# Optimization experiments

Hardware: AMD Instinct MI355X
Metric: run time of the kernel (lower is better)

The kernel has to match this reference:

```python
import jax, jax.numpy as jnp
import numpy as np

B, N, E, H = 2, 50000, 400000, 128


def _lin_init(k, fan_in, fan_out):
    s = 1.0 / np.sqrt(fan_in)
    kw, kb = jax.random.split(k)
    W = jax.random.uniform(kw, (fan_in, fan_out), jnp.float32, -s, s)
    b = jax.random.uniform(kb, (fan_out,), jnp.float32, -s, s)
    return W, b


def setup_inputs() -> dict:
    key = jax.random.key(0)
    ks = jax.random.split(key, 7)
    x = jax.random.normal(ks[0], (B, N, H), jnp.float32)
    edge_index = jax.random.randint(ks[1], (2, E), 0, N, jnp.int64)
    edge_attr = jax.random.normal(ks[2], (B, E, H), jnp.float32)
    We1, be1 = _lin_init(ks[3], 3 * H, H)
    We2, be2 = _lin_init(ks[4], H, H)
    Wn1, bn1 = _lin_init(ks[5], 2 * H, H)
    Wn2, bn2 = _lin_init(ks[6], H, H)
    return dict(x=x, edge_index=edge_index, edge_attr=edge_attr,
                We1=We1, be1=be1, We2=We2, be2=be2,
                Wn1=Wn1, bn1=bn1, Wn2=Wn2, bn2=bn2)


def reference(x, edge_index, edge_attr, We1, be1, We2, be2, Wn1, bn1, Wn2, bn2):
    src = edge_index[0]
    dest = edge_index[1]
    # edge model: MLP(concat(src_feat, dest_feat, edge_attr))  [B,E,3H] -> [B,E,H]
    m = jnp.concatenate([x[:, src], x[:, dest], edge_attr], axis=-1)
    e = jax.nn.relu(m @ We1 + be1) @ We2 + be2
    # node model: scatter-sum messages to dest nodes, then MLP(concat(x, agg))
    agg = jax.vmap(lambda eb: jax.ops.segment_sum(eb, dest, num_segments=x.shape[1]))(e)
    h = jnp.concatenate([x, agg], axis=-1)  # [B,N,2H]
    x_out = jax.nn.relu(h @ Wn1 + bn1) @ Wn2 + bn2
    return x_out, e
```

## Files before the change

### kernel.cpp

```cpp
#include <hip/hip_runtime.h>
#include <hip/hip_bf16.h>

#define Hd 128
#define Nn 50000
#define Ee 400000
#define Bb 2
#define NROWS 100000
#define TPB2 3125
#define NT2 6250

typedef __attribute__((ext_vector_type(8))) short bf16x8;
typedef __attribute__((ext_vector_type(4))) short bf16x4;
typedef __attribute__((ext_vector_type(4))) float f32x4;

static __device__ __forceinline__ short f2bf(float f) {
    __hip_bfloat16 h = __float2bfloat16(f);
    return *reinterpret_cast<short*>(&h);
}
static __device__ __forceinline__ float bf2f(short s) {
    union { unsigned u; float f; } v; v.u = ((unsigned)(unsigned short)s) << 16;
    return v.f;
}
static __device__ __forceinline__ bf16x8 cvt8(float4 a, float4 b) {
    bf16x8 r;
    r[0] = f2bf(a.x); r[1] = f2bf(a.y); r[2] = f2bf(a.z); r[3] = f2bf(a.w);
    r[4] = f2bf(b.x); r[5] = f2bf(b.y); r[6] = f2bf(b.z); r[7] = f2bf(b.w);
    return r;
}
static __device__ __forceinline__ unsigned pk2(float a, float b) {
    return (unsigned)(unsigned short)f2bf(a) | ((unsigned)(unsigned short)f2bf(b) << 16);
}
static __device__ __forceinline__ void lds_barrier() {
    asm volatile("s_waitcnt lgkmcnt(0)" ::: "memory");
    __builtin_amdgcn_s_barrier();
}

__global__ void prep_weights(const float* __restrict__ We1, const float* __restrict__ We2,
                             const float* __restrict__ Wn1, const float* __restrict__ Wn2,
                             short* __restrict__ wbuf) {
    int gid = blockIdx.x * 256 + threadIdx.x;
    if (gid < 32768) {
        int c = gid >> 7, k = gid & 127;
        float v = (c < 128) ? We1[k * 128 + c] : We1[(k + 128) * 128 + (c - 128)];
        wbuf[gid] = f2bf(v); return;
    }
    int g = gid - 32768;
    if (g < 16384) { int c = g >> 7, k = g & 127; wbuf[gid] = f2bf(We1[(k + 256) * 128 + c]); return; }
    g -= 16384;
    if (g < 16384) { int c = g >> 7, k = g & 127; wbuf[gid] = f2bf(We2[k * 128 + c]); return; }
    g -= 16384;
    if (g < 32768) { int c = g >> 8, k = g & 255; wbuf[gid] = f2bf(Wn1[k * 128 + c]); return; }
    g -= 32768;
    if (g < 16384) { int c = g >> 7, k = g & 127; wbuf[gid] = f2bf(Wn2[k * 128 + c]); }
}

__global__ void hist_kernel(const int* __restrict__ ei, int* __restrict__ cnt) {
    int t = blockIdx.x * 256 + threadIdx.x;
    if (t < Ee) atomicAdd(&cnt[ei[Ee + t]], 1);
}
__global__ void scan1(const int* __restrict__ cnt, int* __restrict__ cur, int* __restrict__ part) {
    __shared__ int s[256];
    int i = blockIdx.x * 256 + threadIdx.x;
    int v = (i < Nn) ? cnt[i] : 0;
    s[threadIdx.x] = v; __syncthreads();
    #pragma unroll
    for (int off = 1; off < 256; off <<= 1) {
        int u = (threadIdx.x >= off) ? s[threadIdx.x - off] : 0;
        __syncthreads(); s[threadIdx.x] += u; __syncthreads();
    }
    if (i < Nn) cur[i] = s[threadIdx.x] - v;
    if (threadIdx.x == 255) part[blockIdx.x] = s[255];
}
__global__ void scan2(int* __restrict__ part) {
    if (threadIdx.x == 0 && blockIdx.x == 0) {
        int run = 0;
        for (int i = 0; i < 196; i++) { int t = part[i]; part[i] = run; run += t; }
    }
}
__global__ void scan3(int* __restrict__ cur, const int* __restrict__ part) {
    int i = blockIdx.x * 256 + threadIdx.x;
    if (i < Nn) cur[i] += part[blockIdx.x];
}
__global__ void scatter_k(const int* __restrict__ ei, int* __restrict__ cur, int* __restrict__ elist) {
    int t = blockIdx.x * 256 + threadIdx.x;
    if (t < Ee) { int d = ei[Ee + t]; int pos = atomicAdd(&cur[d], 1); elist[pos] = t; }
}

__global__ __launch_bounds__(256) void node_pre(
    const float* __restrict__ x, const short* __restrict__ WabT,
    short* __restrict__ xa, short* __restrict__ xb)
{
    __shared__ __align__(16) short X[32 * 128];

    const int nbase = blockIdx.x * 32;
    const int t = threadIdx.x;
    const int wv = t >> 6, lane = t & 63;
    const int row16 = lane & 15, kg = lane >> 4;

    {
        int g = t >> 3, q = t & 7;
        const float* src = x + ((size_t)(nbase + g)) * Hd + q * 16;
        float4 a0 = ((const float4*)src)[0], a1 = ((const float4*)src)[1];
        float4 a2 = ((const float4*)src)[2], a3 = ((const float4*)src)[3];
        ((bf16x8*)X)[g * 16 + ((q * 2) ^ (g & 7))]     = cvt8(a0, a1);
        ((bf16x8*)X)[g * 16 + ((q * 2 + 1) ^ (g & 7))] = cvt8(a2, a3);
    }

    bf16x8 wf[4][4];
    #pragma unroll
    for (int nt = 0; nt < 4; nt++) {
        int n = wv * 64 + nt * 16 + row16;
        #pragma unroll
        for (int kt = 0; kt < 4; kt++)
            wf[kt][nt] = *(const bf16x8*)(WabT + n * 128 + kt * 32 + kg * 8);
    }
    __syncthreads();

    f32x4 acc[2][4];
    #pragma unroll
    for (int mt = 0; mt < 2; mt++)
        #pragma unroll
        for (int nt = 0; nt < 4; nt++) acc[mt][nt] = (f32x4){0.f,0.f,0.f,0.f};

    #pragma unroll
    for (int mt = 0; mt < 2; mt++) {
        int row = mt * 16 + row16;
        #pragma unroll
        for (int kt = 0; kt < 4; kt++) {
            bf16x8 xf = ((const bf16x8*)X)[row * 16 + ((kt * 4 + kg) ^ (row & 7))];
            #pragma unroll
            for (int nt = 0; nt < 4; nt++)
                acc[mt][nt] = __builtin_amdgcn_mfma_f32_16x16x32_bf16(wf[kt][nt], xf, acc[mt][nt], 0, 0, 0);
        }
    }

    #pragma unroll
    for (int mt = 0; mt < 2; mt++) {
        size_t node = nbase + mt * 16 + row16;
        #pragma unroll
        for (int nt = 0; nt < 4; nt++) {
            int ch = wv * 64 + nt * 16 + kg * 4;
            uint2 pk = { pk2(acc[mt][nt][0], acc[mt][nt][1]), pk2(acc[mt][nt][2], acc[mt][nt][3]) };
            short* dst = (ch < 128) ? (xa + node * Hd + ch) : (xb + node * Hd + (ch - 128));
            *(uint2*)dst = pk;
        }
    }
}

__global__ __launch_bounds__(512) void edge_mlp(
    const float* __restrict__ ea, const int* __restrict__ ei,
    const int* __restrict__ elist,
    const short* __restrict__ xa, const short* __restrict__ xb,
    const short* __restrict__ W1cT, const float* __restrict__ be1,
    const short* __restrict__ W2T, const float* __restrict__ be2,
    float* __restrict__ e_out, float* __restrict__ agg)
{
    __shared__ __align__(16) char smem[65536 + 1536];
    short* Aea = (short*)smem;
    short* A2  = (short*)(smem + 32768);
    int* ol = (int*)(smem + 65536);
    int* sl = ol + 128;
    int* dl = sl + 128;

    const int orig = blockIdx.x;
    const int q = NT2 / 8, rr = NT2 % 8;
    const int xcd = orig & 7, idx = orig >> 3;
    const int tile = (xcd < rr ? xcd * (q + 1) : rr * (q + 1) + (xcd - rr) * q) + idx;

    const int b = tile / TPB2;
    const int w0 = (tile % TPB2) * 128;
    const int t = threadIdx.x;
    const int wv = t >> 6, lane = t & 63;
    const int row16 = lane & 15, kg = lane >> 4;
    const int n0 = wv * 16 + kg * 4;
    const int sr = t >> 3, sq = t & 7;

    if (t < 128) {
        int o = elist[w0 + t];
        ol[t] = o; sl[t] = ei[o]; dl[t] = ei[Ee + o];
    }
    __syncthreads();

    int on[8], sn[8], dn[8];
    #pragma unroll
    for (int mt = 0; mt < 8; mt++) {
        int r = mt * 16 + row16;
        on[mt] = ol[r]; sn[mt] = sl[r]; dn[mt] = dl[r];
    }

    #pragma unroll
    for (int h = 0; h < 2; h++) {
        int row = sr + h * 64;
        const float* src = ea + ((size_t)b * Ee + ol[row]) * Hd + sq * 16;
        float4 a0 = ((const float4*)src)[0], a1 = ((const float4*)src)[1];
        float4 a2 = ((const float4*)src)[2], a3 = ((const float4*)src)[3];
        ((bf16x8*)Aea)[row * 16 + ((sq * 2) ^ (row & 7))]     = cvt8(a0, a1);
        ((bf16x8*)Aea)[row * 16 + ((sq * 2 + 1) ^ (row & 7))] = cvt8(a2, a3);
    }

    bf16x8 w1[4], w2[4];
    {
        const short* wp1 = W1cT + (wv * 16 + row16) * 128 + kg * 8;
        const short* wp2 = W2T  + (wv * 16 + row16) * 128 + kg * 8;
        #pragma unroll
        for (int kt = 0; kt < 4; kt++) {
            w1[kt] = *(const bf16x8*)(wp1 + kt * 32);
            w2[kt] = *(const bf16x8*)(wp2 + kt * 32);
        }
    }
    bf16x4 av[8], bv[8];
    #pragma unroll
    for (int mt = 0; mt < 8; mt++) {
        av[mt] = *(const bf16x4*)(xa + ((size_t)b * Nn + sn[mt]) * Hd + n0);
        bv[mt] = *(const bf16x4*)(xb + ((size_t)b * Nn + dn[mt]) * Hd + n0);
    }
    const float4 b1v = *(const float4*)(be1 + n0);
    const float4 b2v = *(const float4*)(be2 + n0);
    lds_barrier();

    f32x4 acc[8];
    #pragma unroll
    for (int mt = 0; mt < 8; mt++) acc[mt] = (f32x4){0.f,0.f,0.f,0.f};
    #pragma unroll
    for (int kt = 0; kt < 4; kt++) {
        #pragma unroll
        for (int mt = 0; mt < 8; mt++) {
            int row = mt * 16 + row16;
            bf16x8 af = ((const bf16x8*)Aea)[row * 16 + ((kt * 4 + kg) ^ (row & 7))];
            acc[mt] = __builtin_amdgcn_mfma_f32_16x16x32_bf16(w1[kt], af, acc[mt], 0, 0, 0);
        }
    }

    #pragma unroll
    for (int mt = 0; mt < 8; mt++) {
        int row = mt * 16 + row16;
        float vv[4];
        #pragma unroll
        for (int r = 0; r < 4; r++) {
            float u = acc[mt][r] + b1v[r] + bf2f(av[mt][r]) + bf2f(bv[mt][r]);
            vv[r] = u > 0.f ? u : 0.f;
        }
        int G = (n0 >> 3) ^ (row & 7);
        *(uint2*)((char*)A2 + row * 256 + G * 16 + (n0 & 7) * 2) =
            (uint2){ pk2(vv[0], vv[1]), pk2(vv[2], vv[3]) };
    }
    lds_barrier();

    #pragma unroll
    for (int mt = 0; mt < 8; mt++) acc[mt] = (f32x4){0.f,0.f,0.f,0.f};
    #pragma unroll
    for (int kt = 0; kt < 4; kt++) {
        #pragma unroll
        for (int mt = 0; mt < 8; mt++) {
            int row = mt * 16 + row16;
            bf16x8 hf = *(const bf16x8*)((const char*)A2 + row * 256 + (((kt * 4 + kg) ^ (row & 7)) * 16));
            acc[mt] = __builtin_amdgcn_mfma_f32_16x16x32_bf16(w2[kt], hf, acc[mt], 0, 0, 0);
        }
    }

    #pragma unroll
    for (int mt = 0; mt < 8; mt++) {
        acc[mt][0] += b2v.x; acc[mt][1] += b2v.y;
        acc[mt][2] += b2v.z; acc[mt][3] += b2v.w;
        float4 ov = { acc[mt][0], acc[mt][1], acc[mt][2], acc[mt][3] };
        *(float4*)(e_out + ((size_t)b * Ee + on[mt]) * Hd + n0) = ov;
    }
    lds_barrier();

    #pragma unroll
    for (int mt = 0; mt < 8; mt++) {
        int row = mt * 16 + row16;
        float4 ov = { acc[mt][0], acc[mt][1], acc[mt][2], acc[mt][3] };
        *(float4*)(smem + row * 512 + (((n0 >> 2) ^ (row & 7)) << 4)) = ov;
    }
    lds_barrier();

    {
        int c = t & 127, rg2 = t >> 7;
        int g_c = c >> 2, sub = (c & 3) << 2;
        int base = rg2 * 32;
        float s = 0.f;
        int pd = dl[base];
        #pragma unroll
        for (int i = 0; i < 32; i++) {
            int row = base + i;
            float v = *(const float*)(smem + row * 512 + ((g_c ^ (row & 7)) << 4) + sub);
            int d = dl[row];
            if (d != pd) {
                unsafeAtomicAdd(agg + ((size_t)b * Nn + pd) * Hd + c, s);
                s = 0.f; pd = d;
            }
            s += v;
        }
        unsafeAtomicAdd(agg + ((size_t)b * Nn + pd) * Hd + c, s);
    }
}

__global__ __launch_bounds__(512, 4) void node_mlp(
    const float* __restrict__ x, const float* __restrict__ agg,
    const short* __restrict__ Wn1T, const float* __restrict__ bn1,
    const short* __restrict__ Wn2T, const float* __restrict__ bn2,
    float* __restrict__ xout)
{
    __shared__ __align__(16) short A[32 * 256];
    __shared__ __align__(16) short A2[32 * 128];

    const int tilesPerB = (Nn + 31) / 32;
    const int bid = blockIdx.x;
    const int b = bid / tilesPerB;
    const int nbase = (bid % tilesPerB) * 32;
    const int t = threadIdx.x;
    const int wv = t >> 6, lane = t & 63;
    const int row16 = lane & 15, kg = lane >> 4;
    const int n0 = wv * 16 + kg * 4;

    {
        int g = t >> 4, q2 = t & 15;
        int n = nbase + g;
        float4 xv0 = {0,0,0,0}, xv1 = xv0;
        float4 s0 = {0,0,0,0}, s1 = s0;
        if (n < Nn) {
            const float* xr = x + ((size_t)b * Nn + n) * Hd + q2 * 8;
            xv0 = ((const float4*)xr)[0]; xv1 = ((const float4*)xr)[1];
            const float* ar = agg + ((size_t)b * Nn + n) * Hd + q2 * 8;
            s0 = ((const float4*)ar)[0]; s1 = ((const float4*)ar)[1];
        }
        ((bf16x8*)A)[g * 32 + (q2 ^ (g & 7))]        = cvt8(xv0, xv1);
        ((bf16x8*)A)[g * 32 + ((16 + q2) ^ (g & 7))] = cvt8(s0, s1);
    }

    bf16x8 w1[8];
    {
        const short* wp = Wn1T + (wv * 16 + row16) * 256 + kg * 8;
        #pragma unroll
        for (int kt = 0; kt < 8; kt++) w1[kt] = *(const bf16x8*)(wp + kt * 32);
    }
    __syncthreads();

    f32x4 acc[2];
    acc[0] = (f32x4){0.f,0.f,0.f,0.f}; acc[1] = (f32x4){0.f,0.f,0.f,0.f};
    #pragma unroll
    for (int kt = 0; kt < 8; kt++) {
        #pragma unroll
        for (int mt = 0; mt < 2; mt++) {
            int row = mt * 16 + row16;
            bf16x8 af = ((const bf16x8*)A)[row * 32 + ((kt * 4 + kg) ^ (row & 7))];
            acc[mt] = __builtin_amdgcn_mfma_f32_16x16x32_bf16(w1[kt], af, acc[mt], 0, 0, 0);
        }
    }

    float4 b1v = *(const float4*)(bn1 + n0);
    bf16x8 w2[4];
    {
        const short* wp = Wn2T + (wv * 16 + row16) * 128 + kg * 8;
        #pragma unroll
        for (int kt = 0; kt < 4; kt++) w2[kt] = *(const bf16x8*)(wp + kt * 32);
    }

    #pragma unroll
    for (int mt = 0; mt < 2; mt++) {
        int row = mt * 16 + row16;
        float v[4];
        #pragma unroll
        for (int r = 0; r < 4; r++) {
            float u = acc[mt][r] + b1v[r];
            v[r] = u > 0.f ? u : 0.f;
        }
        int G = (n0 >> 3) ^ (row & 7);
        *(uint2*)((char*)A2 + row * 256 + G * 16 + (n0 & 7) * 2) = (uint2){ pk2(v[0], v[1]), pk2(v[2], v[3]) };
    }
    __syncthreads();

    f32x4 acc2[2];
    acc2[0] = (f32x4){0.f,0.f,0.f,0.f}; acc2[1] = (f32x4){0.f,0.f,0.f,0.f};
    #pragma unroll
    for (int kt = 0; kt < 4; kt++) {
        #pragma unroll
        for (int mt = 0; mt < 2; mt++) {
            int row = mt * 16 + row16;
            bf16x8 hf = *(const bf16x8*)((const char*)A2 + row * 256 + (((kt * 4 + kg) ^ (row & 7)) * 16));
            acc2[mt] = __builtin_amdgcn_mfma_f32_16x16x32_bf16(w2[kt], hf, acc2[mt], 0, 0, 0);
        }
    }
    float4 b2v = *(const float4*)(bn2 + n0);
    #pragma unroll
    for (int mt = 0; mt < 2; mt++) {
        int node = nbase + mt * 16 + row16;
        if (node < Nn) {
            float4 ov;
            ov.x = acc2[mt][0] + b2v.x;
            ov.y = acc2[mt][1] + b2v.y;
            ov.z = acc2[mt][2] + b2v.z;
            ov.w = acc2[mt][3] + b2v.w;
            *(float4*)(xout + ((size_t)b * Nn + node) * Hd + n0) = ov;
        }
    }
}

extern "C" void kernel_launch(void* const* d_in, const int* in_sizes, int n_in,
                              void* d_out, int out_size, void* d_ws, size_t ws_size,
                              hipStream_t stream) {
    const float* x   = (const float*)d_in[0];
    const int*   ei  = (const int*)d_in[1];
    const float* ea  = (const float*)d_in[2];
    const float* We1 = (const float*)d_in[3];
    const float* be1 = (const float*)d_in[4];
    const float* We2 = (const float*)d_in[5];
    const float* be2 = (const float*)d_in[6];
    const float* Wn1 = (const float*)d_in[7];
    const float* bn1 = (const float*)d_in[8];
    const float* Wn2 = (const float*)d_in[9];
    const float* bn2 = (const float*)d_in[10];

    float* xout  = (float*)d_out;
    float* e_out = xout + (size_t)Bb * Nn * Hd;

    char* w = (char*)d_ws;
    short* wbuf  = (short*)w;
    short* xa    = (short*)(w + 229376);
    short* xb    = xa + (size_t)NROWS * Hd;
    float* agg   = (float*)(xb + (size_t)NROWS * Hd);
    int*   cnt   = (int*)(agg + (size_t)Bb * Nn * Hd);
    int*   cur   = cnt + Nn;
    int*   part  = cur + Nn;
    int*   elist = part + 256;

    hipMemsetAsync(cnt, 0, Nn * sizeof(int), stream);
    hipMemsetAsync(agg, 0, (size_t)Bb * Nn * Hd * sizeof(float), stream);

    prep_weights<<<448, 256, 0, stream>>>(We1, We2, Wn1, Wn2, wbuf);
    hist_kernel<<<(Ee + 255) / 256, 256, 0, stream>>>(ei, cnt);
    scan1<<<196, 256, 0, stream>>>(cnt, cur, part);
    scan2<<<1, 64, 0, stream>>>(part);
    scan3<<<196, 256, 0, stream>>>(cur, part);
    scatter_k<<<(Ee + 255) / 256, 256, 0, stream>>>(ei, cur, elist);

    node_pre<<<NROWS / 32, 256, 0, stream>>>(x, wbuf, xa, xb);

    edge_mlp<<<NT2, 512, 0, stream>>>(
        ea, ei, elist, xa, xb, wbuf + 32768, be1, wbuf + 49152, be2, e_out, agg);

    node_mlp<<<Bb * ((Nn + 31) / 32), 512, 0, stream>>>(
        x, agg, wbuf + 65536, bn1, wbuf + 98304, bn2, xout);
}
```

Before: 453.8 us.

## Fuse scan stages into scatter and enlarge node MLP tile to 64 rows

Replaces the serial single-thread partial-sum scan with a parallel block scan and folds the block-offset add into the scatter kernel, removing one launch and a pass over the counts. The node MLP now processes 64 nodes per block instead of 32, so each wave's register-held weight fragments are reused across twice as many MFMA tiles and fewer blocks are launched. The larger tile doubles shared memory per block and accumulator registers, and the occupancy hint on launch_bounds is dropped. Out-of-range node loads are clamped rather than zero-filled.

```diff
diff --git a/kernel.cpp b/kernel.cpp
--- a/kernel.cpp
+++ b/kernel.cpp
@@ -72,18 +72,25 @@
     if (threadIdx.x == 255) part[blockIdx.x] = s[255];
 }
 __global__ void scan2(int* __restrict__ part) {
-    if (threadIdx.x == 0 && blockIdx.x == 0) {
-        int run = 0;
-        for (int i = 0; i < 196; i++) { int t = part[i]; part[i] = run; run += t; }
-    }
-}
-__global__ void scan3(int* __restrict__ cur, const int* __restrict__ part) {
-    int i = blockIdx.x * 256 + threadIdx.x;
-    if (i < Nn) cur[i] += part[blockIdx.x];
-}
-__global__ void scatter_k(const int* __restrict__ ei, int* __restrict__ cur, int* __restrict__ elist) {
+    __shared__ int s[256];
+    int i = threadIdx.x;
+    int v = (i < 196) ? part[i] : 0;
+    s[i] = v; __syncthreads();
+    #pragma unroll
+    for (int off = 1; off < 256; off <<= 1) {
+        int u = (i >= off) ? s[i - off] : 0;
+        __syncthreads(); s[i] += u; __syncthreads();
+    }
+    if (i < 196) part[i] = s[i] - v;
+}
+__global__ void scatter_k(const int* __restrict__ ei, int* __restrict__ cur,
+                          const int* __restrict__ part, int* __restrict__ elist) {
     int t = blockIdx.x * 256 + threadIdx.x;
-    if (t < Ee) { int d = ei[Ee + t]; int pos = atomicAdd(&cur[d], 1); elist[pos] = t; }
+    if (t < Ee) {
+        int d = ei[Ee + t];
+        int pos = part[d >> 8] + atomicAdd(&cur[d], 1);
+        elist[pos] = t;
+    }
 }
 
 __global__ __launch_bounds__(256) void node_pre(
@@ -296,37 +303,38 @@
     }
 }
 
-__global__ __launch_bounds__(512, 4) void node_mlp(
+__global__ __launch_bounds__(512) void node_mlp(
     const float* __restrict__ x, const float* __restrict__ agg,
     const short* __restrict__ Wn1T, const float* __restrict__ bn1,
     const short* __restrict__ Wn2T, const float* __restrict__ bn2,
     float* __restrict__ xout)
 {
-    __shared__ __align__(16) short A[32 * 256];
-    __shared__ __align__(16) short A2[32 * 128];
-
-    const int tilesPerB = (Nn + 31) / 32;
+    __shared__ __align__(16) short A[64 * 256];
+    __shared__ __align__(16) short A2[64 * 128];
+
+    const int tilesPerB = (Nn + 63) / 64;
     const int bid = blockIdx.x;
     const int b = bid / tilesPerB;
-    const int nbase = (bid % tilesPerB) * 32;
+    const int nbase = (bid % tilesPerB) * 64;
     const int t = threadIdx.x;
     const int wv = t >> 6, lane = t & 63;
     const int row16 = lane & 15, kg = lane >> 4;
     const int n0 = wv * 16 + kg * 4;
 
     {
-        int g = t >> 4, q2 = t & 15;
+        int g = t >> 3, q = t & 7;
         int n = nbase + g;
-        float4 xv0 = {0,0,0,0}, xv1 = xv0;
-        float4 s0 = {0,0,0,0}, s1 = s0;
-        if (n < Nn) {
-            const float* xr = x + ((size_t)b * Nn + n) * Hd + q2 * 8;
-            xv0 = ((const float4*)xr)[0]; xv1 = ((const float4*)xr)[1];
-            const float* ar = agg + ((size_t)b * Nn + n) * Hd + q2 * 8;
-            s0 = ((const float4*)ar)[0]; s1 = ((const float4*)ar)[1];
-        }
-        ((bf16x8*)A)[g * 32 + (q2 ^ (g & 7))]        = cvt8(xv0, xv1);
-        ((bf16x8*)A)[g * 32 + ((16 + q2) ^ (g & 7))] = cvt8(s0, s1);
+        int nc_ = n < Nn ? n : Nn - 1;
+        const float* xr = x + ((size_t)b * Nn + nc_) * Hd + q * 16;
+        float4 x0 = ((const float4*)xr)[0], x1 = ((const float4*)xr)[1];
+        float4 x2 = ((const float4*)xr)[2], x3 = ((const float4*)xr)[3];
+        const float* ar = agg + ((size_t)b * Nn + nc_) * Hd + q * 16;
+        float4 s0 = ((const float4*)ar)[0], s1 = ((const float4*)ar)[1];
+        float4 s2 = ((const float4*)ar)[2], s3 = ((const float4*)ar)[3];
+        ((bf16x8*)A)[g * 32 + ((q * 2) ^ (g & 7))]          = cvt8(x0, x1);
+        ((bf16x8*)A)[g * 32 + ((q * 2 + 1) ^ (g & 7))]      = cvt8(x2, x3);
+        ((bf16x8*)A)[g * 32 + ((16 + q * 2) ^ (g & 7))]     = cvt8(s0, s1);
+        ((bf16x8*)A)[g * 32 + ((16 + q * 2 + 1) ^ (g & 7))] = cvt8(s2, s3);
     }
 
     bf16x8 w1[8];
@@ -335,21 +343,22 @@
         #pragma unroll
         for (int kt = 0; kt < 8; kt++) w1[kt] = *(const bf16x8*)(wp + kt * 32);
     }
-    __syncthreads();
-
-    f32x4 acc[2];
-    acc[0] = (f32x4){0.f,0.f,0.f,0.f}; acc[1] = (f32x4){0.f,0.f,0.f,0.f};
+    const float4 b1v = *(const float4*)(bn1 + n0);
+    lds_barrier();
+
+    f32x4 acc[4];
+    #pragma unroll
+    for (int mt = 0; mt < 4; mt++) acc[mt] = (f32x4){0.f,0.f,0.f,0.f};
     #pragma unroll
     for (int kt = 0; kt < 8; kt++) {
         #pragma unroll
-        for (int mt = 0; mt < 2; mt++) {
+        for (int mt = 0; mt < 4; mt++) {
             int row = mt * 16 + row16;
             bf16x8 af = ((const bf16x8*)A)[row * 32 + ((kt * 4 + kg) ^ (row & 7))];
             acc[mt] = __builtin_amdgcn_mfma_f32_16x16x32_bf16(w1[kt], af, acc[mt], 0, 0, 0);
         }
     }
 
-    float4 b1v = *(const float4*)(bn1 + n0);
     bf16x8 w2[4];
     {
         const short* wp = Wn2T + (wv * 16 + row16) * 128 + kg * 8;
@@ -358,7 +367,7 @@
     }
 
     #pragma unroll
-    for (int mt = 0; mt < 2; mt++) {
+    for (int mt = 0; mt < 4; mt++) {
         int row = mt * 16 + row16;
         float v[4];
         #pragma unroll
@@ -369,29 +378,29 @@
         int G = (n0 >> 3) ^ (row & 7);
         *(uint2*)((char*)A2 + row * 256 + G * 16 + (n0 & 7) * 2) = (uint2){ pk2(v[0], v[1]), pk2(v[2], v[3]) };
     }
-    __syncthreads();
-
-    f32x4 acc2[2];
-    acc2[0] = (f32x4){0.f,0.f,0.f,0.f}; acc2[1] = (f32x4){0.f,0.f,0.f,0.f};
+    lds_barrier();
+
+    #pragma unroll
+    for (int mt = 0; mt < 4; mt++) acc[mt] = (f32x4){0.f,0.f,0.f,0.f};
     #pragma unroll
     for (int kt = 0; kt < 4; kt++) {
         #pragma unroll
-        for (int mt = 0; mt < 2; mt++) {
+        for (int mt = 0; mt < 4; mt++) {
             int row = mt * 16 + row16;
             bf16x8 hf = *(const bf16x8*)((const char*)A2 + row * 256 + (((kt * 4 + kg) ^ (row & 7)) * 16));
-            acc2[mt] = __builtin_amdgcn_mfma_f32_16x16x32_bf16(w2[kt], hf, acc2[mt], 0, 0, 0);
-        }
-    }
-    float4 b2v = *(const float4*)(bn2 + n0);
-    #pragma unroll
-    for (int mt = 0; mt < 2; mt++) {
+            acc[mt] = __builtin_amdgcn_mfma_f32_16x16x32_bf16(w2[kt], hf, acc[mt], 0, 0, 0);
+        }
+    }
+    const float4 b2v = *(const float4*)(bn2 + n0);
+    #pragma unroll
+    for (int mt = 0; mt < 4; mt++) {
         int node = nbase + mt * 16 + row16;
         if (node < Nn) {
             float4 ov;
-            ov.x = acc2[mt][0] + b2v.x;
-            ov.y = acc2[mt][1] + b2v.y;
-            ov.z = acc2[mt][2] + b2v.z;
-            ov.w = acc2[mt][3] + b2v.w;
+            ov.x = acc[mt][0] + b2v.x;
+            ov.y = acc[mt][1] + b2v.y;
+            ov.z = acc[mt][2] + b2v.z;
+            ov.w = acc[mt][3] + b2v.w;
             *(float4*)(xout + ((size_t)b * Nn + node) * Hd + n0) = ov;
         }
     }
@@ -431,15 +440,14 @@
     prep_weights<<<448, 256, 0, stream>>>(We1, We2, Wn1, Wn2, wbuf);
     hist_kernel<<<(Ee + 255) / 256, 256, 0, stream>>>(ei, cnt);
     scan1<<<196, 256, 0, stream>>>(cnt, cur, part);
-    scan2<<<1, 64, 0, stream>>>(part);
-    scan3<<<196, 256, 0, stream>>>(cur, part);
-    scatter_k<<<(Ee + 255) / 256, 256, 0, stream>>>(ei, cur, elist);
+    scan2<<<1, 256, 0, stream>>>(part);
+    scatter_k<<<(Ee + 255) / 256, 256, 0, stream>>>(ei, cur, part, elist);
 
     node_pre<<<NROWS / 32, 256, 0, stream>>>(x, wbuf, xa, xb);
 
     edge_mlp<<<NT2, 512, 0, stream>>>(
         ea, ei, elist, xa, xb, wbuf + 32768, be1, wbuf + 49152, be2, e_out, agg);
 
-    node_mlp<<<Bb * ((Nn + 31) / 32), 512, 0, stream>>>(
+    node_mlp<<<Bb * ((Nn + 63) / 64), 512, 0, stream>>>(
         x, agg, wbuf + 65536, bn1, wbuf + 98304, bn2, xout);
 }
```

New measurement: 436.7 us. 1.04x faster.
